# Kernel optimization log

Hardware: AMD Instinct MI355X
Metric: run time of the kernel (lower is better)

Reference implementation:

```python
import jax, jax.numpy as jnp
import numpy as np

NUM_NEURONS = 2048
EMBED_DIM = 1024
WINDOW_SIZES = np.array([1, 2, 4, 8, 16, 32, 64, 128, 256, 512, 1024, 2048], dtype=np.int32)
WINDOW_MAX = 2048
TEMPERATURE = 1.0


def setup_inputs() -> dict:
    key = jax.random.key(0)
    ks = jax.random.split(key, 12)
    W = len(WINDOW_SIZES)
    inp = {
        "x": jax.random.normal(ks[0], (8192, EMBED_DIM), dtype=jnp.float32),
        "n_weights": jax.random.normal(ks[1], (NUM_NEURONS, EMBED_DIM), dtype=jnp.float32) * 0.01,
        "n_biases": jnp.zeros((NUM_NEURONS,), dtype=jnp.float32),
        "combo_w": jax.random.normal(ks[2], (W, NUM_NEURONS, NUM_NEURONS), dtype=jnp.float32) * (1.0 / np.sqrt(NUM_NEURONS)),
        "combo_b": jax.random.normal(ks[3], (W, NUM_NEURONS), dtype=jnp.float32) * 0.01,
        "q_w": jax.random.normal(ks[4], (EMBED_DIM, NUM_NEURONS), dtype=jnp.float32) * (1.0 / np.sqrt(NUM_NEURONS)),
        "q_b": jnp.zeros((EMBED_DIM,), dtype=jnp.float32),
        "k_w": jax.random.normal(ks[5], (EMBED_DIM, NUM_NEURONS), dtype=jnp.float32) * (1.0 / np.sqrt(NUM_NEURONS)),
        "k_b": jnp.zeros((EMBED_DIM,), dtype=jnp.float32),
        "cerebellum": jnp.ones((W,), dtype=jnp.float32),
        "judge_bias": jnp.zeros((W,), dtype=jnp.float32),
        "credibility_bias": jnp.zeros((W,), dtype=jnp.float32),
        "parliament_blend": jnp.float32(0.5),
    }
    return inp


def _forward(x, n_weights, n_biases, combo_w, combo_b, q_w, q_b, k_w, k_b,
             cerebellum, judge_bias, credibility_bias, parliament_blend):
    # NEURON forward: [S, E] @ [E, N] + [N] -> tanh -> clamp
    act = jnp.clip(jnp.tanh(x @ n_weights.T + n_biases), -5.0, 5.0)  # [S, N]
    S = act.shape[0]
    tail = min(S, WINDOW_MAX)
    # faithful replication of stackedWindowMeans: last `tail` activations go to the
    # END of a [WINDOW_MAX, N] buffer, mask selects the FIRST windowSize rows
    padded = jnp.zeros((WINDOW_MAX, NUM_NEURONS), dtype=act.dtype).at[WINDOW_MAX - tail:].set(act[S - tail:])
    wsz = jnp.asarray(WINDOW_SIZES, dtype=jnp.float32)  # [W]
    mask = (jnp.arange(WINDOW_MAX)[None, :] < jnp.asarray(WINDOW_SIZES)[:, None]).astype(act.dtype)  # [W, WINDOW_MAX]
    window_out = (mask @ padded) / wsz[:, None]  # [W, N]
    # per-window Linear combos (torch Linear: y = x @ W.T + b)
    combo = jnp.einsum('wn,wmn->wm', window_out, combo_w) + combo_b  # [W, N]
    query = combo @ q_w.T + q_b + (judge_bias * cerebellum)[:, None]  # [W, E]
    key = window_out @ k_w.T + k_b + (credibility_bias * cerebellum)[:, None]  # [W, E]
    scores = (query @ key.T) / TEMPERATURE  # [W, W]
    # selfScores + peerScores == column sums of scores
    combined_scores = scores.sum(axis=0)  # [W]
    pb = jax.nn.sigmoid(parliament_blend)
    blended = ((1.0 - pb) * cerebellum + pb * combined_scores) * cerebellum
    combined_window_weights = jax.nn.softmax(blended)  # [W]
    ctx = jnp.sum(combo + combined_window_weights[:, None], axis=0, keepdims=True)  # [1, N]
    ctx = ctx + 0.2 * combo.mean(axis=0, keepdims=True)
    return ctx


def reference(x, n_weights, n_biases, combo_w, combo_b, q_w, q_b, k_w, k_b,
              cerebellum, judge_bias, credibility_bias, parliament_blend):
    return _forward(x, n_weights, n_biases, combo_w, combo_b, q_w, q_b, k_w, k_b,
                    cerebellum, judge_bias, credibility_bias, parliament_blend)
```

## Files before the change

kernel.cpp:

```cpp
#include <hip/hip_runtime.h>
#include <hip/hip_bf16.h>
#include <math.h>

#define N_NEUR 2048
#define EMB 1024
#define S_TOT 8192
#define WMAX 2048
#define NW 12

typedef __attribute__((ext_vector_type(8))) short bf16x8;
typedef __attribute__((ext_vector_type(4))) float f32x4;
typedef __attribute__((ext_vector_type(4))) int int4v;

__device__ inline short f2bf(float f) {
    union { float f; unsigned u; } v; v.f = f;
    unsigned r = v.u + 0x7FFFu + ((v.u >> 16) & 1u);
    return (short)(r >> 16);
}

__global__ __launch_bounds__(256) void precast(const float* __restrict__ xt,
                                               const float* __restrict__ nw,
                                               short* __restrict__ A,
                                               short* __restrict__ W) {
    const int HALF = (N_NEUR * EMB) / 4;
    int g = blockIdx.x * 256 + threadIdx.x;
    const float4* src; short* dst;
    if (g < HALF) { src = (const float4*)xt; dst = A; }
    else          { g -= HALF; src = (const float4*)nw; dst = W; }
    float4 v = src[g];
    short4 o;
    o.x = f2bf(v.x); o.y = f2bf(v.y); o.z = f2bf(v.z); o.w = f2bf(v.w);
    *(short4*)(dst + (size_t)g * 4) = o;
}

#define LDK 72

__global__ __launch_bounds__(256) void gemm_seg(const short* __restrict__ A,
                                                const short* __restrict__ W,
                                                const float* __restrict__ bias,
                                                float* __restrict__ seg) {
    __shared__ short As[64 * LDK];
    __shared__ short Bs[64 * LDK];
    const int t = threadIdx.x;
    const int bm = blockIdx.y, bn = blockIdx.x;
    const int lane = t & 63, wid = t >> 6;
    const int wr = wid >> 1, wc = wid & 1;
    const int l15 = lane & 15, lhi = lane >> 4;
    const int srow = t >> 2, scol = (t & 3) * 16;
    const short* gA = A + (size_t)(bm * 64 + srow) * EMB + scol;
    const short* gW = W + (size_t)(bn * 64 + srow) * EMB + scol;
    short* wA = &As[srow * LDK + scol];
    short* wB = &Bs[srow * LDK + scol];
    f32x4 acc[2][2] = {};
    for (int k0 = 0; k0 < EMB; k0 += 64) {
        __syncthreads();
        int4v a0 = *(const int4v*)(gA + k0);
        int4v a1 = *(const int4v*)(gA + k0 + 8);
        int4v b0 = *(const int4v*)(gW + k0);
        int4v b1 = *(const int4v*)(gW + k0 + 8);
        *(int4v*)wA = a0; *(int4v*)(wA + 8) = a1;
        *(int4v*)wB = b0; *(int4v*)(wB + 8) = b1;
        __syncthreads();
        bf16x8 af[2][2], bb[2][2];
        #pragma unroll
        for (int kk = 0; kk < 2; ++kk) {
            #pragma unroll
            for (int m = 0; m < 2; ++m)
                af[kk][m] = *(const bf16x8*)&As[(wr * 32 + m * 16 + l15) * LDK + kk * 32 + lhi * 8];
            #pragma unroll
            for (int n = 0; n < 2; ++n)
                bb[kk][n] = *(const bf16x8*)&Bs[(wc * 32 + n * 16 + l15) * LDK + kk * 32 + lhi * 8];
        }
        #pragma unroll
        for (int kk = 0; kk < 2; ++kk)
            #pragma unroll
            for (int m = 0; m < 2; ++m)
                #pragma unroll
                for (int n = 0; n < 2; ++n)
                    acc[m][n] = __builtin_amdgcn_mfma_f32_16x16x32_bf16(af[kk][m], bb[kk][n], acc[m][n], 0, 0, 0);
    }
    if (bm > 0) {
        int jseg = 38 - __clz(bm);
        #pragma unroll
        for (int n = 0; n < 2; ++n) {
            int col = bn * 64 + wc * 32 + n * 16 + l15;
            float bc = bias[col];
            float s = 0.f;
            #pragma unroll
            for (int m = 0; m < 2; ++m)
                #pragma unroll
                for (int j = 0; j < 4; ++j)
                    s += tanhf(acc[m][n][j] + bc);
            s += __shfl_xor(s, 16);
            s += __shfl_xor(s, 32);
            if (lhi == 0) atomicAdd(&seg[jseg * N_NEUR + col], s);
        }
    } else {
        #pragma unroll
        for (int n = 0; n < 2; ++n) {
            int col = bn * 64 + wc * 32 + n * 16 + l15;
            float bc = bias[col];
            if (wr == 1) {
                float s = 0.f;
                #pragma unroll
                for (int m = 0; m < 2; ++m)
                    #pragma unroll
                    for (int j = 0; j < 4; ++j)
                        s += tanhf(acc[m][n][j] + bc);
                s += __shfl_xor(s, 16);
                s += __shfl_xor(s, 32);
                if (lhi == 0) atomicAdd(&seg[6 * N_NEUR + col], s);
            } else {
                float s = 0.f;
                #pragma unroll
                for (int j = 0; j < 4; ++j)
                    s += tanhf(acc[1][n][j] + bc);
                s += __shfl_xor(s, 16);
                s += __shfl_xor(s, 32);
                if (lhi == 0) atomicAdd(&seg[5 * N_NEUR + col], s);
                #pragma unroll
                for (int j = 0; j < 4; ++j) {
                    int r = lhi * 4 + j;
                    int sj = (r == 0) ? 0 : (32 - __clz(r));
                    atomicAdd(&seg[sj * N_NEUR + col], tanhf(acc[0][n][j] + bc));
                }
            }
        }
    }
}

__global__ __launch_bounds__(256) void winout(const float* __restrict__ seg,
                                              float* __restrict__ wout) {
    int n = blockIdx.x * 256 + threadIdx.x;
    float run = 0.f;
    #pragma unroll
    for (int w = 0; w < NW; ++w) {
        run += seg[w * N_NEUR + n];
        wout[w * N_NEUR + n] = run * (1.0f / (float)(1 << w));
    }
}

__global__ __launch_bounds__(256) void combo_dot(const float* __restrict__ cw,
                                                 const float* __restrict__ wout,
                                                 float* __restrict__ acc) {
    int wid = threadIdx.x >> 6, lane = threadIdx.x & 63;
    int r = blockIdx.x * 4 + wid;
    int w = r >> 11, m = r & 2047;
    const float4* row  = (const float4*)(cw + (size_t)(w * N_NEUR + m) * N_NEUR);
    const float4* wrow = (const float4*)(wout + w * N_NEUR);
    float s = 0.f;
    #pragma unroll
    for (int i = 0; i < 8; ++i) {
        float4 a = row[i * 64 + lane];
        float4 b = wrow[i * 64 + lane];
        s += a.x * b.x + a.y * b.y + a.z * b.z + a.w * b.w;
    }
    #pragma unroll
    for (int off = 32; off > 0; off >>= 1) s += __shfl_down(s, off);
    if (lane == 0) atomicAdd(&acc[m], s);
}

__global__ __launch_bounds__(256) void finalize(const float* __restrict__ acc,
                                                const float* __restrict__ cb,
                                                float* __restrict__ out) {
    int m = blockIdx.x * 256 + threadIdx.x;
    float bs = 0.f;
    #pragma unroll
    for (int w = 0; w < NW; ++w) bs += cb[w * N_NEUR + m];
    out[m] = 1.0166666666666666f * (acc[m] + bs) + 1.0f;
}

extern "C" void kernel_launch(void* const* d_in, const int* in_sizes, int n_in,
                              void* d_out, int out_size, void* d_ws, size_t ws_size,
                              hipStream_t stream) {
    const float* x  = (const float*)d_in[0];
    const float* nw = (const float*)d_in[1];
    const float* nb = (const float*)d_in[2];
    const float* cw = (const float*)d_in[3];
    const float* cb = (const float*)d_in[4];
    float* out = (float*)d_out;

    char* ws = (char*)d_ws;
    float* acc  = (float*)ws;
    float* seg  = (float*)(ws + 8192);
    float* wout = (float*)(ws + 8192 + 98304);
    short* Abf  = (short*)(ws + 204800);
    short* Wbf  = (short*)(ws + 204800 + 4194304);

    hipMemsetAsync(ws, 0, 106496, stream);

    precast<<<4096, 256, 0, stream>>>(x + (size_t)(S_TOT - WMAX) * EMB, nw, Abf, Wbf);

    dim3 g1(32, 32);
    gemm_seg<<<g1, 256, 0, stream>>>(Abf, Wbf, nb, seg);

    winout<<<8, 256, 0, stream>>>(seg, wout);

    combo_dot<<<6144, 256, 0, stream>>>(cw, wout, acc);

    finalize<<<8, 256, 0, stream>>>(acc, cb, out);
}
```

Measured before the change: 68.24 us.

## Double-buffer GEMM tiles via direct global-to-LDS loads and fold finalize into combo

The GEMM now loads tiles straight from global memory into LDS with global_load_lds into two alternating buffers, prefetching the next K-slice while MFMAs run on the current one. It uses an XOR swizzle in place of padding to avoid bank conflicts and raises wave priority around the MFMA block. The finalize kernel is removed: the bias sum and output initialization move into the winout kernel, and combo_dot atomically adds its scaled partials straight into the output. This cuts one launch and one memset region, at the cost of double LDS use and more complex swizzled indexing.

Result: faster. 61.67 us (-9.6%).

```diff
diff --git a/kernel.cpp b/kernel.cpp
--- a/kernel.cpp
+++ b/kernel.cpp
@@ -10,7 +10,6 @@
 
 typedef __attribute__((ext_vector_type(8))) short bf16x8;
 typedef __attribute__((ext_vector_type(4))) float f32x4;
-typedef __attribute__((ext_vector_type(4))) int int4v;
 
 __device__ inline short f2bf(float f) {
     union { float f; unsigned u; } v; v.f = f;
@@ -33,44 +32,62 @@
     *(short4*)(dst + (size_t)g * 4) = o;
 }
 
-#define LDK 72
+#define GLDS(g, l) __builtin_amdgcn_global_load_lds(                          \
+    (const __attribute__((address_space(1))) void*)(g),                       \
+    (__attribute__((address_space(3))) void*)(l), 16, 0, 0)
 
 __global__ __launch_bounds__(256) void gemm_seg(const short* __restrict__ A,
                                                 const short* __restrict__ W,
                                                 const float* __restrict__ bias,
                                                 float* __restrict__ seg) {
-    __shared__ short As[64 * LDK];
-    __shared__ short Bs[64 * LDK];
+    __shared__ short As[2][64 * 64];
+    __shared__ short Bs[2][64 * 64];
     const int t = threadIdx.x;
     const int bm = blockIdx.y, bn = blockIdx.x;
     const int lane = t & 63, wid = t >> 6;
     const int wr = wid >> 1, wc = wid & 1;
     const int l15 = lane & 15, lhi = lane >> 4;
-    const int srow = t >> 2, scol = (t & 3) * 16;
-    const short* gA = A + (size_t)(bm * 64 + srow) * EMB + scol;
-    const short* gW = W + (size_t)(bn * 64 + srow) * EMB + scol;
-    short* wA = &As[srow * LDK + scol];
-    short* wB = &Bs[srow * LDK + scol];
+    const int srow = lane >> 3;
+    const int pslot = (lane & 7) ^ srow;
+    const short* gA0 = A + (size_t)(bm * 64 + wid * 16 + 0 + srow) * EMB + pslot * 8;
+    const short* gA1 = A + (size_t)(bm * 64 + wid * 16 + 8 + srow) * EMB + pslot * 8;
+    const short* gB0 = W + (size_t)(bn * 64 + wid * 16 + 0 + srow) * EMB + pslot * 8;
+    const short* gB1 = W + (size_t)(bn * 64 + wid * 16 + 8 + srow) * EMB + pslot * 8;
+    short* lA0[2] = { &As[0][(wid * 16 + 0) * 64], &As[1][(wid * 16 + 0) * 64] };
+    short* lA1[2] = { &As[0][(wid * 16 + 8) * 64], &As[1][(wid * 16 + 8) * 64] };
+    short* lB0[2] = { &Bs[0][(wid * 16 + 0) * 64], &Bs[1][(wid * 16 + 0) * 64] };
+    short* lB1[2] = { &Bs[0][(wid * 16 + 8) * 64], &Bs[1][(wid * 16 + 8) * 64] };
+
     f32x4 acc[2][2] = {};
-    for (int k0 = 0; k0 < EMB; k0 += 64) {
-        __syncthreads();
-        int4v a0 = *(const int4v*)(gA + k0);
-        int4v a1 = *(const int4v*)(gA + k0 + 8);
-        int4v b0 = *(const int4v*)(gW + k0);
-        int4v b1 = *(const int4v*)(gW + k0 + 8);
-        *(int4v*)wA = a0; *(int4v*)(wA + 8) = a1;
-        *(int4v*)wB = b0; *(int4v*)(wB + 8) = b1;
-        __syncthreads();
+
+    GLDS(gA0, lA0[0]); GLDS(gA1, lA1[0]);
+    GLDS(gB0, lB0[0]); GLDS(gB1, lB1[0]);
+    __syncthreads();
+
+    int cur = 0;
+    for (int ks = 0; ks < 16; ++ks) {
+        if (ks < 15) {
+            int k0 = (ks + 1) * 64;
+            GLDS(gA0 + k0, lA0[cur ^ 1]); GLDS(gA1 + k0, lA1[cur ^ 1]);
+            GLDS(gB0 + k0, lB0[cur ^ 1]); GLDS(gB1 + k0, lB1[cur ^ 1]);
+        }
         bf16x8 af[2][2], bb[2][2];
         #pragma unroll
         for (int kk = 0; kk < 2; ++kk) {
             #pragma unroll
-            for (int m = 0; m < 2; ++m)
-                af[kk][m] = *(const bf16x8*)&As[(wr * 32 + m * 16 + l15) * LDK + kk * 32 + lhi * 8];
-            #pragma unroll
-            for (int n = 0; n < 2; ++n)
-                bb[kk][n] = *(const bf16x8*)&Bs[(wc * 32 + n * 16 + l15) * LDK + kk * 32 + lhi * 8];
-        }
+            for (int m = 0; m < 2; ++m) {
+                int row = wr * 32 + m * 16 + l15;
+                int slot = (kk * 4 + lhi) ^ (row & 7);
+                af[kk][m] = *(const bf16x8*)&As[cur][row * 64 + slot * 8];
+            }
+            #pragma unroll
+            for (int n = 0; n < 2; ++n) {
+                int row = wc * 32 + n * 16 + l15;
+                int slot = (kk * 4 + lhi) ^ (row & 7);
+                bb[kk][n] = *(const bf16x8*)&Bs[cur][row * 64 + slot * 8];
+            }
+        }
+        __builtin_amdgcn_s_setprio(1);
         #pragma unroll
         for (int kk = 0; kk < 2; ++kk)
             #pragma unroll
@@ -78,7 +95,11 @@
                 #pragma unroll
                 for (int n = 0; n < 2; ++n)
                     acc[m][n] = __builtin_amdgcn_mfma_f32_16x16x32_bf16(af[kk][m], bb[kk][n], acc[m][n], 0, 0, 0);
-    }
+        __builtin_amdgcn_s_setprio(0);
+        __syncthreads();
+        cur ^= 1;
+    }
+
     if (bm > 0) {
         int jseg = 38 - __clz(bm);
         #pragma unroll
@@ -129,8 +150,10 @@
     }
 }
 
-__global__ __launch_bounds__(256) void winout(const float* __restrict__ seg,
-                                              float* __restrict__ wout) {
+__global__ __launch_bounds__(256) void winout_init(const float* __restrict__ seg,
+                                                   const float* __restrict__ cb,
+                                                   float* __restrict__ wout,
+                                                   float* __restrict__ out) {
     int n = blockIdx.x * 256 + threadIdx.x;
     float run = 0.f;
     #pragma unroll
@@ -138,11 +161,15 @@
         run += seg[w * N_NEUR + n];
         wout[w * N_NEUR + n] = run * (1.0f / (float)(1 << w));
     }
+    float bs = 0.f;
+    #pragma unroll
+    for (int w = 0; w < NW; ++w) bs += cb[w * N_NEUR + n];
+    out[n] = 1.0166666666666666f * bs + 1.0f;
 }
 
 __global__ __launch_bounds__(256) void combo_dot(const float* __restrict__ cw,
                                                  const float* __restrict__ wout,
-                                                 float* __restrict__ acc) {
+                                                 float* __restrict__ out) {
     int wid = threadIdx.x >> 6, lane = threadIdx.x & 63;
     int r = blockIdx.x * 4 + wid;
     int w = r >> 11, m = r & 2047;
@@ -157,17 +184,7 @@
     }
     #pragma unroll
     for (int off = 32; off > 0; off >>= 1) s += __shfl_down(s, off);
-    if (lane == 0) atomicAdd(&acc[m], s);
-}
-
-__global__ __launch_bounds__(256) void finalize(const float* __restrict__ acc,
-                                                const float* __restrict__ cb,
-                                                float* __restrict__ out) {
-    int m = blockIdx.x * 256 + threadIdx.x;
-    float bs = 0.f;
-    #pragma unroll
-    for (int w = 0; w < NW; ++w) bs += cb[w * N_NEUR + m];
-    out[m] = 1.0166666666666666f * (acc[m] + bs) + 1.0f;
+    if (lane == 0) atomicAdd(&out[m], 1.0166666666666666f * s);
 }
 
 extern "C" void kernel_launch(void* const* d_in, const int* in_sizes, int n_in,
@@ -181,22 +198,19 @@
     float* out = (float*)d_out;
 
     char* ws = (char*)d_ws;
-    float* acc  = (float*)ws;
-    float* seg  = (float*)(ws + 8192);
-    float* wout = (float*)(ws + 8192 + 98304);
+    float* seg  = (float*)ws;
+    float* wout = (float*)(ws + 98304);
     short* Abf  = (short*)(ws + 204800);
     short* Wbf  = (short*)(ws + 204800 + 4194304);
 
-    hipMemsetAsync(ws, 0, 106496, stream);
+    hipMemsetAsync(ws, 0, 98304, stream);
 
     precast<<<4096, 256, 0, stream>>>(x + (size_t)(S_TOT - WMAX) * EMB, nw, Abf, Wbf);
 
     dim3 g1(32, 32);
     gemm_seg<<<g1, 256, 0, stream>>>(Abf, Wbf, nb, seg);
 
-    winout<<<8, 256, 0, stream>>>(seg, wout);
-
-    combo_dot<<<6144, 256, 0, stream>>>(cw, wout, acc);
-
-    finalize<<<8, 256, 0, stream>>>(acc, cb, out);
-}
+    winout_init<<<8, 256, 0, stream>>>(seg, cb, wout, out);
+
+    combo_dot<<<6144, 256, 0, stream>>>(cw, wout, out);
+}
```
